# Optimization experiments

Hardware: AMD Instinct MI355X
Metric: run time of the kernel (lower is better)

Reference implementation:

```python
import jax, jax.numpy as jnp
import numpy as np

B, S1, S2, H, H2, D, K = 1, 1024, 8192, 32, 8, 128, 128


def setup_inputs() -> dict:
    key = jax.random.key(0)
    k1, k2, k3, k4 = jax.random.split(key, 4)
    q = jax.random.normal(k1, (B, S1, H, D), dtype=jnp.float16)
    k = jax.random.normal(k2, (B, S2, H2, D), dtype=jnp.float16)
    v = jax.random.normal(k3, (B, S2, H2, D), dtype=jnp.float16)
    sparse_indices = jax.random.randint(k4, (B, S1, H2, K), 0, S2, dtype=jnp.int32)
    return {"q": q, "k": k, "v": v, "sparse_indices": sparse_indices}


def reference(q, k, v, sparse_indices):
    # q: [B,S1,H,D]  k,v: [B,S2,H2,D]  sparse_indices: [B,S1,H2,K]
    b, s1, h, d = q.shape
    h2 = sparse_indices.shape[2]
    g = h // h2  # GQA group size
    scale = 1.0 / np.sqrt(d).astype(np.float32)
    qg = q.reshape(b, s1, h2, g, d)  # group queries per kv head
    b_idx = jnp.arange(b)[:, None, None, None]
    h_idx = jnp.arange(h2)[None, None, :, None]
    # gather per-query sparse KV sets: [B,S1,H2,K,D]
    kg = k[b_idx, sparse_indices, h_idx]
    vg = v[b_idx, sparse_indices, h_idx]
    scores = jnp.einsum('bshgd,bshkd->bshgk', qg, kg).astype(jnp.float32) * scale
    p = jax.nn.softmax(scores, axis=-1).astype(q.dtype)
    out = jnp.einsum('bshgk,bshkd->bshgd', p, vg)  # [B,S1,H2,G,D]
    return out.reshape(b, s1, h, d).astype(jnp.float16)
```

## Files before the change

### kernel.cpp

```cpp
#include <hip/hip_runtime.h>
#include <stdint.h>
#include <math.h>

#define NH 32
#define NH2 8
#define DD 128
#define KSEL 128
#define GG 4
#define S2MASK 8191
#define KVELTS (8192 * NH2 * DD)

typedef _Float16 h8   __attribute__((ext_vector_type(8)));
typedef _Float16 h2t  __attribute__((ext_vector_type(2)));
typedef __fp16   hp2  __attribute__((ext_vector_type(2)));
typedef float    f32x4 __attribute__((ext_vector_type(4)));

static __device__ __forceinline__ h8 cvt8(float4 a, float4 b) {
  union { h8 v; hp2 p[4]; } u;
  u.p[0] = __builtin_amdgcn_cvt_pkrtz(a.x, a.y);
  u.p[1] = __builtin_amdgcn_cvt_pkrtz(a.z, a.w);
  u.p[2] = __builtin_amdgcn_cvt_pkrtz(b.x, b.y);
  u.p[3] = __builtin_amdgcn_cvt_pkrtz(b.z, b.w);
  return u.v;
}

__global__ __launch_bounds__(256) void convert_kv(
    const float4* __restrict__ kf, const float4* __restrict__ vf,
    ushort4* __restrict__ kh, ushort4* __restrict__ vh, int n4) {
  int i = blockIdx.x * blockDim.x + threadIdx.x;
  const int stride = gridDim.x * blockDim.x;
  union { ushort4 u; hp2 p[2]; } ua;
  for (; i < n4; i += stride) {
    float4 a = kf[i];
    ua.p[0] = __builtin_amdgcn_cvt_pkrtz(a.x, a.y);
    ua.p[1] = __builtin_amdgcn_cvt_pkrtz(a.z, a.w);
    kh[i] = ua.u;
    float4 b = vf[i];
    ua.p[0] = __builtin_amdgcn_cvt_pkrtz(b.x, b.y);
    ua.p[1] = __builtin_amdgcn_cvt_pkrtz(b.z, b.w);
    vh[i] = ua.u;
  }
}

#define WAVE_FENCE() asm volatile("" ::: "memory")

__global__ __launch_bounds__(256) void sparse_attn_f16(
    const float* __restrict__ q, const _Float16* __restrict__ kh,
    const _Float16* __restrict__ vh, const int* __restrict__ idx,
    float* __restrict__ out) {
  __shared__ int sOff[4][KSEL];
  __shared__ __align__(16) float sP[4][KSEL][GG];

  const int tid = threadIdx.x;
  const int w = tid >> 6;
  const int lane = tid & 63;
  const int h2 = blockIdx.x & 7;
  const int s1 = ((blockIdx.x >> 3) << 2) + w;

  const int* ip = idx + (s1 * NH2 + h2) * KSEL;
  sOff[w][lane]      = (ip[lane]      & S2MASK) * (NH2 * DD);
  sOff[w][lane + 64] = (ip[lane + 64] & S2MASK) * (NH2 * DD);

  const int m  = lane & 15;
  const int kg = lane >> 4;

  h8 aq[4];
#pragma unroll
  for (int t = 0; t < 4; ++t)
#pragma unroll
    for (int i = 0; i < 8; ++i) aq[t][i] = (_Float16)0;
  if (m < GG) {
    const float* qp = q + (s1 * NH + h2 * GG + m) * DD + kg * 8;
#pragma unroll
    for (int t = 0; t < 4; ++t) {
      float4 f0 = *(const float4*)(qp + 32 * t);
      float4 f1 = *(const float4*)(qp + 32 * t + 4);
      aq[t] = cvt8(f0, f1);
    }
  }

  WAVE_FENCE();

  const float scale = 0.08838834764831845f;

#pragma unroll 2
  for (int nt = 0; nt < 8; ++nt) {
    const _Float16* kp = kh + sOff[w][nt * 16 + m] + h2 * DD + kg * 8;
    f32x4 acc = {0.f, 0.f, 0.f, 0.f};
#pragma unroll
    for (int t = 0; t < 4; ++t) {
      h8 bk = *(const h8*)(kp + 32 * t);
      acc = __builtin_amdgcn_mfma_f32_16x16x32_f16(aq[t], bk, acc, 0, 0, 0);
    }
    if (lane < 16) {
      float4 sc = make_float4(acc[0] * scale, acc[1] * scale,
                              acc[2] * scale, acc[3] * scale);
      *(float4*)&sP[w][nt * 16 + lane][0] = sc;
    }
  }

  WAVE_FENCE();

  {
    float4 p0 = *(const float4*)&sP[w][lane][0];
    float4 p1 = *(const float4*)&sP[w][lane + 64][0];
    float4 mx = make_float4(fmaxf(p0.x, p1.x), fmaxf(p0.y, p1.y),
                            fmaxf(p0.z, p1.z), fmaxf(p0.w, p1.w));
#pragma unroll
    for (int off = 1; off < 64; off <<= 1) {
      mx.x = fmaxf(mx.x, __shfl_xor(mx.x, off));
      mx.y = fmaxf(mx.y, __shfl_xor(mx.y, off));
      mx.z = fmaxf(mx.z, __shfl_xor(mx.z, off));
      mx.w = fmaxf(mx.w, __shfl_xor(mx.w, off));
    }
    float4 e0 = make_float4(__expf(p0.x - mx.x), __expf(p0.y - mx.y),
                            __expf(p0.z - mx.z), __expf(p0.w - mx.w));
    float4 e1 = make_float4(__expf(p1.x - mx.x), __expf(p1.y - mx.y),
                            __expf(p1.z - mx.z), __expf(p1.w - mx.w));
    float4 sm = make_float4(e0.x + e1.x, e0.y + e1.y, e0.z + e1.z, e0.w + e1.w);
#pragma unroll
    for (int off = 1; off < 64; off <<= 1) {
      sm.x += __shfl_xor(sm.x, off);
      sm.y += __shfl_xor(sm.y, off);
      sm.z += __shfl_xor(sm.z, off);
      sm.w += __shfl_xor(sm.w, off);
    }
    float4 inv = make_float4(1.f / fmaxf(sm.x, 1e-30f), 1.f / fmaxf(sm.y, 1e-30f),
                             1.f / fmaxf(sm.z, 1e-30f), 1.f / fmaxf(sm.w, 1e-30f));
    *(float4*)&sP[w][lane][0] =
        make_float4(e0.x * inv.x, e0.y * inv.y, e0.z * inv.z, e0.w * inv.w);
    *(float4*)&sP[w][lane + 64][0] =
        make_float4(e1.x * inv.x, e1.y * inv.y, e1.z * inv.z, e1.w * inv.w);
  }

  WAVE_FENCE();

  float a00 = 0.f, a01 = 0.f, a10 = 0.f, a11 = 0.f;
  float a20 = 0.f, a21 = 0.f, a30 = 0.f, a31 = 0.f;
  const _Float16* vb = vh + h2 * DD + lane * 2;
#pragma unroll
  for (int ch = 0; ch < 4; ++ch) {
    h2t vv[32];
#pragma unroll
    for (int j = 0; j < 32; ++j)
      vv[j] = *(const h2t*)(vb + sOff[w][ch * 32 + j]);
#pragma unroll
    for (int j = 0; j < 32; ++j) {
      const float4 p = *(const float4*)&sP[w][ch * 32 + j][0];
      const float vx = (float)vv[j][0];
      const float vy = (float)vv[j][1];
      a00 = fmaf(p.x, vx, a00); a01 = fmaf(p.x, vy, a01);
      a10 = fmaf(p.y, vx, a10); a11 = fmaf(p.y, vy, a11);
      a20 = fmaf(p.z, vx, a20); a21 = fmaf(p.z, vy, a21);
      a30 = fmaf(p.w, vx, a30); a31 = fmaf(p.w, vy, a31);
    }
  }

  float* op = out + (s1 * NH + h2 * GG) * DD + lane * 2;
  *(float2*)(op + 0 * DD) = make_float2(a00, a01);
  *(float2*)(op + 1 * DD) = make_float2(a10, a11);
  *(float2*)(op + 2 * DD) = make_float2(a20, a21);
  *(float2*)(op + 3 * DD) = make_float2(a30, a31);
}

__global__ __launch_bounds__(256) void sparse_attn_f32(
    const float* __restrict__ q, const float* __restrict__ k,
    const float* __restrict__ v, const int* __restrict__ idx,
    float* __restrict__ out) {
  __shared__ int sIdx[4][KSEL];
  __shared__ __align__(16) float sP[4][KSEL][GG];

  const int tid = threadIdx.x;
  const int w = tid >> 6;
  const int lane = tid & 63;
  const int h2 = blockIdx.x & 7;
  const int s1 = ((blockIdx.x >> 3) << 2) + w;

  const int* ip = idx + (s1 * NH2 + h2) * KSEL;
  sIdx[w][lane]      = ip[lane] & S2MASK;
  sIdx[w][lane + 64] = ip[lane + 64] & S2MASK;

  const int m  = lane & 15;
  const int kg = lane >> 4;

  h8 aq[4];
#pragma unroll
  for (int t = 0; t < 4; ++t)
#pragma unroll
    for (int i = 0; i < 8; ++i) aq[t][i] = (_Float16)0;
  if (m < GG) {
    const float* qp = q + (s1 * NH + h2 * GG + m) * DD + kg * 8;
#pragma unroll
    for (int t = 0; t < 4; ++t) {
      float4 f0 = *(const float4*)(qp + 32 * t);
      float4 f1 = *(const float4*)(qp + 32 * t + 4);
      aq[t] = cvt8(f0, f1);
    }
  }
  __syncthreads();

  const float scale = 0.08838834764831845f;
#pragma unroll 2
  for (int nt = 0; nt < 8; ++nt) {
    const int s2 = sIdx[w][nt * 16 + m];
    const float* kp = k + (s2 * NH2 + h2) * DD + kg * 8;
    f32x4 acc = {0.f, 0.f, 0.f, 0.f};
#pragma unroll
    for (int t = 0; t < 4; ++t) {
      float4 f0 = *(const float4*)(kp + 32 * t);
      float4 f1 = *(const float4*)(kp + 32 * t + 4);
      acc = __builtin_amdgcn_mfma_f32_16x16x32_f16(aq[t], cvt8(f0, f1), acc, 0, 0, 0);
    }
    if (lane < 16) {
      float4 sc = make_float4(acc[0] * scale, acc[1] * scale,
                              acc[2] * scale, acc[3] * scale);
      *(float4*)&sP[w][nt * 16 + lane][0] = sc;
    }
  }
  __syncthreads();

  {
    float4 p0 = *(const float4*)&sP[w][lane][0];
    float4 p1 = *(const float4*)&sP[w][lane + 64][0];
    float4 mx = make_float4(fmaxf(p0.x, p1.x), fmaxf(p0.y, p1.y),
                            fmaxf(p0.z, p1.z), fmaxf(p0.w, p1.w));
#pragma unroll
    for (int off = 1; off < 64; off <<= 1) {
      mx.x = fmaxf(mx.x, __shfl_xor(mx.x, off));
      mx.y = fmaxf(mx.y, __shfl_xor(mx.y, off));
      mx.z = fmaxf(mx.z, __shfl_xor(mx.z, off));
      mx.w = fmaxf(mx.w, __shfl_xor(mx.w, off));
    }
    float4 e0 = make_float4(__expf(p0.x - mx.x), __expf(p0.y - mx.y),
                            __expf(p0.z - mx.z), __expf(p0.w - mx.w));
    float4 e1 = make_float4(__expf(p1.x - mx.x), __expf(p1.y - mx.y),
                            __expf(p1.z - mx.z), __expf(p1.w - mx.w));
    float4 sm = make_float4(e0.x + e1.x, e0.y + e1.y, e0.z + e1.z, e0.w + e1.w);
#pragma unroll
    for (int off = 1; off < 64; off <<= 1) {
      sm.x += __shfl_xor(sm.x, off);
      sm.y += __shfl_xor(sm.y, off);
      sm.z += __shfl_xor(sm.z, off);
      sm.w += __shfl_xor(sm.w, off);
    }
    float4 inv = make_float4(1.f / fmaxf(sm.x, 1e-30f), 1.f / fmaxf(sm.y, 1e-30f),
                             1.f / fmaxf(sm.z, 1e-30f), 1.f / fmaxf(sm.w, 1e-30f));
    *(float4*)&sP[w][lane][0] =
        make_float4(e0.x * inv.x, e0.y * inv.y, e0.z * inv.z, e0.w * inv.w);
    *(float4*)&sP[w][lane + 64][0] =
        make_float4(e1.x * inv.x, e1.y * inv.y, e1.z * inv.z, e1.w * inv.w);
  }
  __syncthreads();

  float a00 = 0.f, a01 = 0.f, a10 = 0.f, a11 = 0.f;
  float a20 = 0.f, a21 = 0.f, a30 = 0.f, a31 = 0.f;
  const float* vb = v + h2 * DD + lane * 2;
#pragma unroll 8
  for (int j = 0; j < KSEL; ++j) {
    const int s2 = sIdx[w][j];
    const float2 vv = *(const float2*)(vb + (size_t)s2 * (NH2 * DD));
    const float4 p = *(const float4*)&sP[w][j][0];
    a00 = fmaf(p.x, vv.x, a00); a01 = fmaf(p.x, vv.y, a01);
    a10 = fmaf(p.y, vv.x, a10); a11 = fmaf(p.y, vv.y, a11);
    a20 = fmaf(p.z, vv.x, a20); a21 = fmaf(p.z, vv.y, a21);
    a30 = fmaf(p.w, vv.x, a30); a31 = fmaf(p.w, vv.y, a31);
  }

  float* op = out + (s1 * NH + h2 * GG) * DD + lane * 2;
  *(float2*)(op + 0 * DD) = make_float2(a00, a01);
  *(float2*)(op + 1 * DD) = make_float2(a10, a11);
  *(float2*)(op + 2 * DD) = make_float2(a20, a21);
  *(float2*)(op + 3 * DD) = make_float2(a30, a31);
}

extern "C" void kernel_launch(void* const* d_in, const int* in_sizes, int n_in,
                              void* d_out, int out_size, void* d_ws, size_t ws_size,
                              hipStream_t stream) {
  const float* q = (const float*)d_in[0];
  const float* k = (const float*)d_in[1];
  const float* v = (const float*)d_in[2];
  const int* idx = (const int*)d_in[3];
  float* out = (float*)d_out;

  const size_t need = (size_t)2 * KVELTS * sizeof(_Float16);
  if (ws_size >= need) {
    _Float16* kh = (_Float16*)d_ws;
    _Float16* vh = kh + KVELTS;
    convert_kv<<<dim3(2048), dim3(256), 0, stream>>>(
        (const float4*)k, (const float4*)v,
        (ushort4*)kh, (ushort4*)vh, KVELTS / 4);
    sparse_attn_f16<<<dim3(2048), dim3(256), 0, stream>>>(q, kh, vh, idx, out);
  } else {
    sparse_attn_f32<<<dim3(2048), dim3(256), 0, stream>>>(q, k, v, idx, out);
  }
}
```

Measured before the change: 170.3 us.

## Restructure PV accumulation to 16-byte V loads with cross-lane reduction

The P·V stage is reorganized so each lane loads 8 contiguous fp16 values of a V row (16 bytes) instead of 2. Each of the four lane quarters handles a different subset of the selected keys, and partial sums are combined with xor shuffles over lanes 16 and 32. This cuts the number of gather load instructions and widens memory transactions. In exchange it uses 32 accumulators per lane, adds shuffle reductions, and indexes acc[r] dynamically at the store, which may force the accumulators into scratch memory.

```diff
diff --git a/kernel.cpp b/kernel.cpp
--- a/kernel.cpp
+++ b/kernel.cpp
@@ -135,32 +135,41 @@
 
   WAVE_FENCE();
 
-  float a00 = 0.f, a01 = 0.f, a10 = 0.f, a11 = 0.f;
-  float a20 = 0.f, a21 = 0.f, a30 = 0.f, a31 = 0.f;
-  const _Float16* vb = vh + h2 * DD + lane * 2;
-#pragma unroll
-  for (int ch = 0; ch < 4; ++ch) {
-    h2t vv[32];
-#pragma unroll
-    for (int j = 0; j < 32; ++j)
-      vv[j] = *(const h2t*)(vb + sOff[w][ch * 32 + j]);
-#pragma unroll
-    for (int j = 0; j < 32; ++j) {
-      const float4 p = *(const float4*)&sP[w][ch * 32 + j][0];
-      const float vx = (float)vv[j][0];
-      const float vy = (float)vv[j][1];
-      a00 = fmaf(p.x, vx, a00); a01 = fmaf(p.x, vy, a01);
-      a10 = fmaf(p.y, vx, a10); a11 = fmaf(p.y, vy, a11);
-      a20 = fmaf(p.z, vx, a20); a21 = fmaf(p.z, vy, a21);
-      a30 = fmaf(p.w, vx, a30); a31 = fmaf(p.w, vy, a31);
-    }
-  }
-
-  float* op = out + (s1 * NH + h2 * GG) * DD + lane * 2;
-  *(float2*)(op + 0 * DD) = make_float2(a00, a01);
-  *(float2*)(op + 1 * DD) = make_float2(a10, a11);
-  *(float2*)(op + 2 * DD) = make_float2(a20, a21);
-  *(float2*)(op + 3 * DD) = make_float2(a30, a31);
+  const int r = kg;
+  const int c = m;
+  float acc[GG][8];
+#pragma unroll
+  for (int g = 0; g < GG; ++g)
+#pragma unroll
+    for (int e = 0; e < 8; ++e) acc[g][e] = 0.f;
+
+  const _Float16* vb = vh + h2 * DD + c * 8;
+#pragma unroll 4
+  for (int ch = 0; ch < 32; ++ch) {
+    const int j = ch * 4 + r;
+    const h8 v8 = *(const h8*)(vb + sOff[w][j]);
+    const float4 p = *(const float4*)&sP[w][j][0];
+#pragma unroll
+    for (int e = 0; e < 8; ++e) {
+      const float vf = (float)v8[e];
+      acc[0][e] = fmaf(p.x, vf, acc[0][e]);
+      acc[1][e] = fmaf(p.y, vf, acc[1][e]);
+      acc[2][e] = fmaf(p.z, vf, acc[2][e]);
+      acc[3][e] = fmaf(p.w, vf, acc[3][e]);
+    }
+  }
+
+#pragma unroll
+  for (int g = 0; g < GG; ++g)
+#pragma unroll
+    for (int e = 0; e < 8; ++e) {
+      acc[g][e] += __shfl_xor(acc[g][e], 16);
+      acc[g][e] += __shfl_xor(acc[g][e], 32);
+    }
+
+  float* op = out + (s1 * NH + h2 * GG + r) * DD + c * 8;
+  *(float4*)(op + 0) = make_float4(acc[r][0], acc[r][1], acc[r][2], acc[r][3]);
+  *(float4*)(op + 4) = make_float4(acc[r][4], acc[r][5], acc[r][6], acc[r][7]);
 }
 
 __global__ __launch_bounds__(256) void sparse_attn_f32(
```

Result: slower. 174.3 us (+2.4%).
